# Kernel tuning notes

Measured on AMD Instinct MI355X. Metric: run time of the kernel, lower is better.

## Reference

```python
import jax, jax.numpy as jnp
import numpy as np

N_NODES = 10000
N_EDGES = 160000
F_IN = 256
HEADS = 4
F_OUT = 256
NEG_SLOPE = 0.2  # PyG GATConv default negative_slope
EPS = 1e-5       # GraphNorm eps


def gat_conv(x, src, dst, W, a_src, a_dst, bias, concat):
    """PyG-style GATConv. x:[N,Fin], W:[Fin,H*C], a_src/a_dst:[H,C], bias:[H*C] or [C].
    src/dst already include self-loops (add_self_loops=True default)."""
    N = x.shape[0]
    H, C = a_src.shape
    h = (x @ W).reshape(N, H, C)                      # per-head projected features
    al_s = jnp.einsum('nhc,hc->nh', h, a_src)          # [N,H]
    al_d = jnp.einsum('nhc,hc->nh', h, a_dst)          # [N,H]
    e = jax.nn.leaky_relu(al_s[src] + al_d[dst], NEG_SLOPE)  # [E,H] raw scores
    # segment softmax over edges grouped by destination node
    m = jax.ops.segment_max(e, dst, num_segments=N)    # [N,H]; every node has a self-loop
    ex = jnp.exp(e - m[dst])
    denom = jax.ops.segment_sum(ex, dst, num_segments=N)
    alpha = ex / denom[dst]                            # [E,H]
    out = jax.ops.segment_sum(h[src] * alpha[:, :, None], dst, num_segments=N)  # [N,H,C]
    out = out.reshape(N, H * C) if concat else out.mean(axis=1)
    return out + bias


def graph_norm(x, w, b, ms):
    """PyG GraphNorm over a single graph: y = w*(x-ms*mean)/sqrt(var+eps)+b."""
    mean = x.mean(axis=0, keepdims=True)
    sh = x - ms * mean
    var = (sh * sh).mean(axis=0, keepdims=True)
    return w * sh / jnp.sqrt(var + EPS) + b


def setup_inputs() -> dict:
    key = jax.random.key(0)
    ks = jax.random.split(key, 12)
    H1 = HEADS * F_IN  # 1024
    s = 0.05
    return {
        'x': jax.random.normal(ks[0], (N_NODES, F_IN), jnp.float32),
        'edge_index': jax.random.randint(ks[1], (2, N_EDGES), 0, N_NODES, jnp.int64),
        'W1': jax.random.normal(ks[2], (F_IN, HEADS * F_IN), jnp.float32) * s,
        'att_src1': jax.random.normal(ks[3], (HEADS, F_IN), jnp.float32) * s,
        'att_dst1': jax.random.normal(ks[4], (HEADS, F_IN), jnp.float32) * s,
        'b1': jnp.zeros((H1,), jnp.float32),
        'gn_w': jnp.ones((H1,), jnp.float32),
        'gn_b': jnp.zeros((H1,), jnp.float32),
        'gn_ms': jnp.ones((H1,), jnp.float32),
        'W2': jax.random.normal(ks[5], (H1, F_OUT), jnp.float32) * s,
        'att_src2': jax.random.normal(ks[6], (1, F_OUT), jnp.float32) * s,
        'att_dst2': jax.random.normal(ks[7], (1, F_OUT), jnp.float32) * s,
        'b2': jnp.zeros((F_OUT,), jnp.float32),
    }


def reference(x, edge_index, W1, att_src1, att_dst1, b1, gn_w, gn_b, gn_ms,
              W2, att_src2, att_dst2, b2):
    N = x.shape[0]
    loop = jnp.arange(N, dtype=edge_index.dtype)
    src = jnp.concatenate([edge_index[0], loop])  # add_self_loops=True
    dst = jnp.concatenate([edge_index[1], loop])
    h = gat_conv(x, src, dst, W1, att_src1, att_dst1, b1, concat=True)   # [N, H*Fin]
    h = graph_norm(h, gn_w, gn_b, gn_ms)
    h = jax.nn.relu(h)
    # F.dropout(training=self.training): eval mode -> identity
    out = gat_conv(h, src, dst, W2, att_src2, att_dst2, b2, concat=False)  # [N, Fout]
    return out
```

## Files before the change

kernel.cpp:

```cpp
#include <hip/hip_runtime.h>
#include <hip/hip_bf16.h>

#define NNODES 10000
#define FIN    256
#define HEADS  4
#define H1DIM  1024
#define FOUT   256
#define NEG    0.2f
#define GNEPS  1e-5f
#define SLOTS  96

typedef unsigned short u16;
typedef __attribute__((ext_vector_type(8))) short bf16x8;
typedef __attribute__((ext_vector_type(4))) float f32x4;

__device__ __forceinline__ float bf2f(u16 u) {
    union { unsigned int i; float f; } v; v.i = ((unsigned int)u) << 16; return v.f;
}
__device__ __forceinline__ u16 f2bf(float f) {
    __hip_bfloat16 h = __float2bfloat16(f);
    union { __hip_bfloat16 h; u16 u; } v; v.h = h; return v.u;
}
__device__ __forceinline__ float lrelu(float v) { return v > 0.f ? v : NEG * v; }

__device__ __forceinline__ void compute_flags(const int* ei, const u16* x,
                                              int& is64, int& isbf)
{
    int or_odd = ei[1] | ei[3] | ei[5] | ei[7] | ei[9] | ei[11];
    is64 = (or_odd == 0) ? 1 : 0;
    int sane = 1;
    for (int i = 0; i < 32; i += 2) {
        u16 w = x[i];
        int e = (w >> 7) & 0xFF;
        if (!(w == 0 || w == 0x8000 || (e >= 100 && e <= 150))) sane = 0;
    }
    isbf = sane;
}

struct CvtDesc { const void* src; float* dst; int n; };
struct CvtTable { CvtDesc d[9]; };

__global__ void pvec_kernel(const void* __restrict__ x, const int* __restrict__ ei,
                            const void* __restrict__ W1,
                            const void* __restrict__ as1, const void* __restrict__ ad1,
                            float* __restrict__ Pm,
                            int* __restrict__ flag, int* __restrict__ fflag)
{
    __shared__ int sfl[2];
    if (threadIdx.x == 0) {
        int is64, isbf;
        compute_flags(ei, (const u16*)x, is64, isbf);
        sfl[0] = is64; sfl[1] = isbf;
        if (blockIdx.x == 0) { flag[0] = is64; fflag[0] = isbf; }
    }
    __syncthreads();
    const int isbf = sfl[1];
    int wave = threadIdx.x >> 6, lane = threadIdx.x & 63;
    int idx = blockIdx.x * 4 + wave;
    int j = idx >> 8, k = idx & 255;
    int hd = j & 3;
    const void* av = (j < 4) ? as1 : ad1;
    int c = lane * 4;
    int widx = k * H1DIM + hd * FIN + c;
    int aidx = hd * FIN + c;
    float wv0, wv1, wv2, wv3, a0, a1, a2, a3;
    if (isbf) {
        ushort4 wu = *reinterpret_cast<const ushort4*>((const u16*)W1 + widx);
        ushort4 au = *reinterpret_cast<const ushort4*>((const u16*)av + aidx);
        wv0 = bf2f(wu.x); wv1 = bf2f(wu.y); wv2 = bf2f(wu.z); wv3 = bf2f(wu.w);
        a0 = bf2f(au.x); a1 = bf2f(au.y); a2 = bf2f(au.z); a3 = bf2f(au.w);
    } else {
        float4 wf = *reinterpret_cast<const float4*>((const float*)W1 + widx);
        float4 af = *reinterpret_cast<const float4*>((const float*)av + aidx);
        wv0 = wf.x; wv1 = wf.y; wv2 = wf.z; wv3 = wf.w;
        a0 = af.x; a1 = af.y; a2 = af.z; a3 = af.w;
    }
    float acc = wv0 * a0 + wv1 * a1 + wv2 * a2 + wv3 * a3;
#pragma unroll
    for (int off = 32; off > 0; off >>= 1)
        acc += __shfl_xor(acc, off, 64);
    if (lane == 0) Pm[j * FIN + k] = acc;
}

#define T0_N 2500
#define T1_N 256
#define T2_N 256
#define T3_N 9
#define T4_N 665
#define PREP_BLOCKS (T0_N + T1_N + T2_N + T3_N + T4_N)

__global__ void prep_kernel(const void* __restrict__ x, const int* __restrict__ ei,
                            const void* __restrict__ W1, const void* __restrict__ W2,
                            CvtTable smalls,
                            u16* __restrict__ xb, u16* __restrict__ W1t,
                            u16* __restrict__ W2t, const float* __restrict__ Pm,
                            int* __restrict__ cursor, int* __restrict__ ssort,
                            float* __restrict__ als, float* __restrict__ ald,
                            int NE, int Etot)
{
    __shared__ int sfl[2];
    __shared__ u16 tile[32][33];
    if (threadIdx.x == 0) {
        int is64, isbf;
        compute_flags(ei, (const u16*)x, is64, isbf);
        sfl[0] = is64; sfl[1] = isbf;
    }
    __syncthreads();
    const int is64 = sfl[0], isbf = sfl[1];
    const int b = blockIdx.x;
    const int tid = threadIdx.x;

    if (b < T0_N) {
        int i4 = (b * 256 + tid) * 4;
        ushort4 o;
        if (isbf) {
            o = *reinterpret_cast<const ushort4*>((const u16*)x + i4);
        } else {
            float4 v = *reinterpret_cast<const float4*>((const float*)x + i4);
            o.x = f2bf(v.x); o.y = f2bf(v.y); o.z = f2bf(v.z); o.w = f2bf(v.w);
        }
        *reinterpret_cast<ushort4*>(xb + i4) = o;
        int wave = tid >> 6, lane = tid & 63;
        int n = b * 4 + wave;
        float x0 = bf2f(o.x), x1 = bf2f(o.y), x2 = bf2f(o.z), x3 = bf2f(o.w);
        float r[8];
#pragma unroll
        for (int j = 0; j < 8; j++) {
            float4 p = *reinterpret_cast<const float4*>(Pm + j * FIN + lane * 4);
            r[j] = x0 * p.x + x1 * p.y + x2 * p.z + x3 * p.w;
        }
#pragma unroll
        for (int off = 32; off > 0; off >>= 1)
#pragma unroll
            for (int j = 0; j < 8; j++)
                r[j] += __shfl_xor(r[j], off, 64);
        if (lane == 0) {
            *reinterpret_cast<float4*>(als + n * 4) = make_float4(r[0], r[1], r[2], r[3]);
            *reinterpret_cast<float4*>(ald + n * 4) = make_float4(r[4], r[5], r[6], r[7]);
        }
    } else if (b < T0_N + T1_N + T2_N) {
        const int task1 = (b < T0_N + T1_N);
        const int bb = task1 ? (b - T0_N) : (b - T0_N - T1_N);
        const void* W = task1 ? W1 : W2;
        u16* Wt = task1 ? W1t : W2t;
        const int K = task1 ? FIN : H1DIM;
        const int N = task1 ? H1DIM : FOUT;
        int ntiles_n = N >> 5;
        int tk = bb / ntiles_n, tn = bb - tk * ntiles_n;
        if (tk >= (K >> 5)) return;
        int k0 = tk << 5, n0 = tn << 5;
        int r = tid >> 5, cdx = tid & 31;
#pragma unroll
        for (int i = 0; i < 4; i++) {
            int kk = i * 8 + r;
            int srcIdx = (k0 + kk) * N + n0 + cdx;
            u16 v = isbf ? ((const u16*)W)[srcIdx] : f2bf(((const float*)W)[srcIdx]);
            tile[kk][cdx] = v;
        }
        __syncthreads();
#pragma unroll
        for (int i = 0; i < 4; i++) {
            int nn = i * 8 + r;
            Wt[(size_t)(n0 + nn) * K + k0 + cdx] = tile[cdx][nn];
        }
    } else if (b < T0_N + T1_N + T2_N + T3_N) {
        const int bb = b - (T0_N + T1_N + T2_N);
        CvtDesc d = smalls.d[bb];
        int i4 = tid * 4;
        if (i4 >= d.n) return;
        if (isbf) {
            ushort4 u = *reinterpret_cast<const ushort4*>((const u16*)d.src + i4);
            *reinterpret_cast<float4*>(d.dst + i4) =
                make_float4(bf2f(u.x), bf2f(u.y), bf2f(u.z), bf2f(u.w));
        } else {
            *reinterpret_cast<float4*>(d.dst + i4) =
                *reinterpret_cast<const float4*>((const float*)d.src + i4);
        }
    } else {
        const int bb = b - (T0_N + T1_N + T2_N + T3_N);
        int e = bb * 256 + tid;
        if (e >= Etot) return;
        int src, dst;
        if (e < NE) {
            src = is64 ? ei[2 * e] : ei[e];
            dst = is64 ? ei[2 * (NE + e)] : ei[NE + e];
        } else {
            src = dst = e - NE;
        }
        if ((unsigned)dst >= NNODES) return;
        if ((unsigned)src >= NNODES) src = 0;
        int idx = atomicAdd(&cursor[dst], 1);
        if (idx < SLOTS) ssort[dst * SLOTS + idx] = src;
    }
}

__global__ void agg_x_kernel(const int* __restrict__ cursor, const int* __restrict__ ssort,
                             const float* __restrict__ als, const float* __restrict__ ald,
                             const u16* __restrict__ xb, u16* __restrict__ zbuf)
{
    const int wave = threadIdx.x >> 6, lane = threadIdx.x & 63;
    const int n = blockIdx.x * 4 + wave;
    const bool active = (n < NNODES);
    int e0 = 0, e1 = 0;
    float4 adv = make_float4(0.f, 0.f, 0.f, 0.f);
    if (active) {
        e0 = n * SLOTS;
        e1 = e0 + min(cursor[n], SLOTS);
        adv = *reinterpret_cast<const float4*>(ald + n * 4);
    }

    float m0 = -1e30f, m1 = -1e30f, m2 = -1e30f, m3 = -1e30f;
    for (int e = e0 + lane; e < e1; e += 64) {
        int s = ssort[e];
        float4 av = *reinterpret_cast<const float4*>(als + s * 4);
        m0 = fmaxf(m0, lrelu(av.x + adv.x));
        m1 = fmaxf(m1, lrelu(av.y + adv.y));
        m2 = fmaxf(m2, lrelu(av.z + adv.z));
        m3 = fmaxf(m3, lrelu(av.w + adv.w));
    }
#pragma unroll
    for (int off = 32; off > 0; off >>= 1) {
        m0 = fmaxf(m0, __shfl_xor(m0, off, 64));
        m1 = fmaxf(m1, __shfl_xor(m1, off, 64));
        m2 = fmaxf(m2, __shfl_xor(m2, off, 64));
        m3 = fmaxf(m3, __shfl_xor(m3, off, 64));
    }

    __shared__ float wlds[4][128][4];
    __shared__ int schk[4];
    int myCh = active ? ((e1 - e0 + 127) >> 7) : 0;
    if (lane == 0) schk[wave] = myCh;
    __syncthreads();
    int mc = max(max(schk[0], schk[1]), max(schk[2], schk[3]));

    float d0 = 0, d1 = 0, d2 = 0, d3 = 0;
    float a[4][4];
#pragma unroll
    for (int h = 0; h < 4; h++)
#pragma unroll
        for (int c = 0; c < 4; c++) a[h][c] = 0.f;

    for (int ch = 0; ch < mc; ch++) {
        int cs = e0 + ch * 128;
        int ce = min(cs + 128, e1);
        if (ch < myCh) {
            for (int e = cs + lane; e < ce; e += 64) {
                int s = ssort[e];
                float4 av = *reinterpret_cast<const float4*>(als + s * 4);
                float w0 = __expf(lrelu(av.x + adv.x) - m0);
                float w1 = __expf(lrelu(av.y + adv.y) - m1);
                float w2 = __expf(lrelu(av.z + adv.z) - m2);
                float w3 = __expf(lrelu(av.w + adv.w) - m3);
                *reinterpret_cast<float4*>(&wlds[wave][e - cs][0]) = make_float4(w0, w1, w2, w3);
                d0 += w0; d1 += w1; d2 += w2; d3 += w3;
            }
        }
        __syncthreads();
        if (ch < myCh) {
            int ee = cs;
            for (; ee + 1 < ce; ee += 2) {
                int s0 = ssort[ee];
                int s1 = ssort[ee + 1];
                float4 w0 = *reinterpret_cast<const float4*>(&wlds[wave][ee - cs][0]);
                float4 w1 = *reinterpret_cast<const float4*>(&wlds[wave][ee + 1 - cs][0]);
                ushort4 xv0 = *reinterpret_cast<const ushort4*>(xb + (size_t)s0 * FIN + lane * 4);
                ushort4 xv1 = *reinterpret_cast<const ushort4*>(xb + (size_t)s1 * FIN + lane * 4);
                float p0 = bf2f(xv0.x), p1 = bf2f(xv0.y), p2 = bf2f(xv0.z), p3 = bf2f(xv0.w);
                a[0][0] += w0.x * p0; a[0][1] += w0.x * p1; a[0][2] += w0.x * p2; a[0][3] += w0.x * p3;
                a[1][0] += w0.y * p0; a[1][1] += w0.y * p1; a[1][2] += w0.y * p2; a[1][3] += w0.y * p3;
                a[2][0] += w0.z * p0; a[2][1] += w0.z * p1; a[2][2] += w0.z * p2; a[2][3] += w0.z * p3;
                a[3][0] += w0.w * p0; a[3][1] += w0.w * p1; a[3][2] += w0.w * p2; a[3][3] += w0.w * p3;
                float q0 = bf2f(xv1.x), q1 = bf2f(xv1.y), q2 = bf2f(xv1.z), q3 = bf2f(xv1.w);
                a[0][0] += w1.x * q0; a[0][1] += w1.x * q1; a[0][2] += w1.x * q2; a[0][3] += w1.x * q3;
                a[1][0] += w1.y * q0; a[1][1] += w1.y * q1; a[1][2] += w1.y * q2; a[1][3] += w1.y * q3;
                a[2][0] += w1.z * q0; a[2][1] += w1.z * q1; a[2][2] += w1.z * q2; a[2][3] += w1.z * q3;
                a[3][0] += w1.w * q0; a[3][1] += w1.w * q1; a[3][2] += w1.w * q2; a[3][3] += w1.w * q3;
            }
            if (ee < ce) {
                int s = ssort[ee];
                float4 w = *reinterpret_cast<const float4*>(&wlds[wave][ee - cs][0]);
                ushort4 xv = *reinterpret_cast<const ushort4*>(xb + (size_t)s * FIN + lane * 4);
                float x0 = bf2f(xv.x), x1 = bf2f(xv.y), x2 = bf2f(xv.z), x3 = bf2f(xv.w);
                a[0][0] += w.x * x0; a[0][1] += w.x * x1; a[0][2] += w.x * x2; a[0][3] += w.x * x3;
                a[1][0] += w.y * x0; a[1][1] += w.y * x1; a[1][2] += w.y * x2; a[1][3] += w.y * x3;
                a[2][0] += w.z * x0; a[2][1] += w.z * x1; a[2][2] += w.z * x2; a[2][3] += w.z * x3;
                a[3][0] += w.w * x0; a[3][1] += w.w * x1; a[3][2] += w.w * x2; a[3][3] += w.w * x3;
            }
        }
        __syncthreads();
    }
    if (!active) return;
#pragma unroll
    for (int off = 32; off > 0; off >>= 1) {
        d0 += __shfl_xor(d0, off, 64);
        d1 += __shfl_xor(d1, off, 64);
        d2 += __shfl_xor(d2, off, 64);
        d3 += __shfl_xor(d3, off, 64);
    }
    float invs[4];
    invs[0] = d0 > 0.f ? 1.f / d0 : 0.f;
    invs[1] = d1 > 0.f ? 1.f / d1 : 0.f;
    invs[2] = d2 > 0.f ? 1.f / d2 : 0.f;
    invs[3] = d3 > 0.f ? 1.f / d3 : 0.f;
#pragma unroll
    for (int h = 0; h < 4; h++) {
        ushort4 o;
        o.x = f2bf(a[h][0] * invs[h]);
        o.y = f2bf(a[h][1] * invs[h]);
        o.z = f2bf(a[h][2] * invs[h]);
        o.w = f2bf(a[h][3] * invs[h]);
        *reinterpret_cast<ushort4*>(zbuf + (size_t)h * NNODES * FIN + (size_t)n * FIN + lane * 4) = o;
    }
}

#define LDS_STRIDE 40
#define KCHUNK2 1024
template<int BM, int BN, int MINW, bool NORM_A, bool BIAS, bool STATS, bool AL2>
__global__ void __launch_bounds__(256, MINW)
mfma_gemm(const u16* __restrict__ A, const u16* __restrict__ Bt,
          u16* __restrict__ C,
          const float* __restrict__ bias,
          float* __restrict__ gsum, float* __restrict__ gsum2,
          const float* __restrict__ gnw, const float* __restrict__ gnb,
          const float* __restrict__ gnms,
          const float* __restrict__ a2s, const float* __restrict__ a2d,
          float* __restrict__ al2s, float* __restrict__ al2d,
          int M, int K, int ldc, long aZ, long bZ, int cZ, int nbx)
{
    constexpr int MI = BM / 32;
    constexpr int NI = BN / 32;
    constexpr int NLOADS = (BM * 4 + BN * 4) / 256;
    __shared__ u16 Alds[BM * LDS_STRIDE];
    __shared__ u16 Blds[BN * LDS_STRIDE];
    __shared__ float sc_lds[NORM_A ? KCHUNK2 : 1];
    __shared__ float sh_lds[NORM_A ? KCHUNK2 : 1];

    int bid = blockIdx.x;
    {
        int nwg = gridDim.x;
        int q = nwg >> 3, r = nwg & 7;
        int xcd = bid & 7, l = bid >> 3;
        bid = (xcd < r ? xcd * (q + 1) : r * (q + 1) + (xcd - r) * q) + l;
    }
    const int bx = bid % nbx;
    const int by = bid / nbx;

    const u16* Az = A + (long)blockIdx.z * aZ;
    const u16* Bz = Bt + (long)blockIdx.z * bZ;

    const int tid  = threadIdx.x;
    const int lane = tid & 63;
    const int wave = tid >> 6;
    const int wm = wave >> 1, wn = wave & 1;
    const int l15 = lane & 15, quad = lane >> 4;
    const int n0 = bx * BN;
    const int m0 = by * BM;

    if (NORM_A) {
        const float invN = 1.0f / (float)NNODES;
        for (int i = tid; i < K; i += 256) {
            float mean = gsum[i] * invN;
            float ex2  = gsum2[i] * invN;
            float msv  = gnms[i];
            float var  = ex2 - 2.f * msv * mean * mean + msv * msv * mean * mean;
            float sc   = gnw[i] * rsqrtf(fmaxf(var, 0.f) + GNEPS);
            sc_lds[i] = sc;
            sh_lds[i] = gnb[i] - sc * msv * mean;
        }
        __syncthreads();
    }

    int lrow[NLOADS], lcol[NLOADS];
    bool lIsA[NLOADS];
#pragma unroll
    for (int i = 0; i < NLOADS; i++) {
        int g = i * 256 + tid;
        lIsA[i] = g < BM * 4;
        int gg = lIsA[i] ? g : g - BM * 4;
        lrow[i] = gg >> 2;
        lcol[i] = (gg & 3) * 8;
    }
    uint4 pre[NLOADS];

    auto issue = [&](int kt) {
#pragma unroll
        for (int i = 0; i < NLOADS; i++) {
            if (lIsA[i]) {
                int gr = m0 + lrow[i];
                pre[i] = (gr < M)
                    ? *reinterpret_cast<const uint4*>(Az + (size_t)gr * K + kt + lcol[i])
                    : make_uint4(0u, 0u, 0u, 0u);
            } else {
                pre[i] = *reinterpret_cast<const uint4*>(Bz + (size_t)(n0 + lrow[i]) * K + kt + lcol[i]);
            }
        }
    };
    auto commit = [&](int kt) {
#pragma unroll
        for (int i = 0; i < NLOADS; i++) {
            uint4 v = pre[i];
            if (lIsA[i]) {
                if (NORM_A) {
                    int kr = kt + lcol[i];
                    float4 s0 = *reinterpret_cast<const float4*>(&sc_lds[kr]);
                    float4 s1 = *reinterpret_cast<const float4*>(&sc_lds[kr + 4]);
                    float4 h0 = *reinterpret_cast<const float4*>(&sh_lds[kr]);
                    float4 h1 = *reinterpret_cast<const float4*>(&sh_lds[kr + 4]);
                    float sc[8] = {s0.x, s0.y, s0.z, s0.w, s1.x, s1.y, s1.z, s1.w};
                    float sh[8] = {h0.x, h0.y, h0.z, h0.w, h1.x, h1.y, h1.z, h1.w};
                    u16* pv = reinterpret_cast<u16*>(&v);
#pragma unroll
                    for (int j = 0; j < 8; j++)
                        pv[j] = f2bf(fmaxf(0.f, bf2f(pv[j]) * sc[j] + sh[j]));
                }
                *reinterpret_cast<uint4*>(&Alds[lrow[i] * LDS_STRIDE + lcol[i]]) = v;
            } else {
                *reinterpret_cast<uint4*>(&Blds[lrow[i] * LDS_STRIDE + lcol[i]]) = v;
            }
        }
    };

    f32x4 acc[MI][NI];
#pragma unroll
    for (int i = 0; i < MI; i++)
#pragma unroll
        for (int j = 0; j < NI; j++) acc[i][j] = (f32x4){0.f, 0.f, 0.f, 0.f};

    issue(0);
    for (int kt = 0; kt < K; kt += 32) {
        commit(kt);
        __syncthreads();
        if (kt + 32 < K) issue(kt + 32);

        bf16x8 a_frag[MI], b_frag[NI];
#pragma unroll
        for (int mi = 0; mi < MI; mi++)
            a_frag[mi] = *reinterpret_cast<const bf16x8*>(
                &Alds[(wm * (BM / 2) + mi * 16 + l15) * LDS_STRIDE + quad * 8]);
#pragma unroll
        for (int ni = 0; ni < NI; ni++)
            b_frag[ni] = *reinterpret_cast<const bf16x8*>(
                &Blds[(wn * (BN / 2) + ni * 16 + l15) * LDS_STRIDE + quad * 8]);
#pragma unroll
        for (int mi = 0; mi < MI; mi++)
#pragma unroll
            for (int ni = 0; ni < NI; ni++)
                acc[mi][ni] = __builtin_amdgcn_mfma_f32_16x16x32_bf16(
                    a_frag[mi], b_frag[ni], acc[mi][ni], 0, 0, 0);
        __syncthreads();
    }

    float sacc[NI], qacc[NI];
#pragma unroll
    for (int ni = 0; ni < NI; ni++) { sacc[ni] = 0.f; qacc[ni] = 0.f; }

#pragma unroll
    for (int mi = 0; mi < MI; mi++) {
#pragma unroll
        for (int r = 0; r < 4; r++) {
            int row = m0 + wm * (BM / 2) + mi * 16 + quad * 4 + r;
            if (row >= M) continue;
            float ps = 0.f, pd = 0.f;
#pragma unroll
            for (int ni = 0; ni < NI; ni++) {
                int col = n0 + wn * (BN / 2) + ni * 16 + l15;
                float v = acc[mi][ni][r];
                if (BIAS) v += bias[blockIdx.z * cZ + col];
                if (STATS) { sacc[ni] += v; qacc[ni] += v * v; }
                if (AL2) { ps += v * a2s[col]; pd += v * a2d[col]; }
                C[(size_t)row * ldc + blockIdx.z * cZ + col] = f2bf(v);
            }
            if (AL2) {
                ps += __shfl_xor(ps, 1, 64); pd += __shfl_xor(pd, 1, 64);
                ps += __shfl_xor(ps, 2, 64); pd += __shfl_xor(pd, 2, 64);
                ps += __shfl_xor(ps, 4, 64); pd += __shfl_xor(pd, 4, 64);
                ps += __shfl_xor(ps, 8, 64); pd += __shfl_xor(pd, 8, 64);
                if (l15 == 0) {
                    atomicAdd(&al2s[row], ps);
                    atomicAdd(&al2d[row], pd);
                }
            }
        }
    }
    if (STATS) {
#pragma unroll
        for (int ni = 0; ni < NI; ni++) {
            float s = sacc[ni], q = qacc[ni];
            s += __shfl_xor(s, 16, 64); q += __shfl_xor(q, 16, 64);
            s += __shfl_xor(s, 32, 64); q += __shfl_xor(q, 32, 64);
            if (quad == 0) {
                int ch = blockIdx.z * cZ + n0 + wn * (BN / 2) + ni * 16 + l15;
                atomicAdd(&gsum[ch], s);
                atomicAdd(&gsum2[ch], q);
            }
        }
    }
}

__global__ void agg2_kernel(const int* __restrict__ cursor, const int* __restrict__ ssort,
                            const float* __restrict__ als, const float* __restrict__ ald,
                            const u16* __restrict__ h2, const float* __restrict__ b2,
                            const int* __restrict__ fflag, void* __restrict__ outv)
{
    const int wave = threadIdx.x >> 6, lane = threadIdx.x & 63;
    const int n = blockIdx.x * 4 + wave;
    const bool active = (n < NNODES);
    int e0 = 0, e1 = 0;
    float adv = 0.f;
    if (active) {
        e0 = n * SLOTS;
        e1 = e0 + min(cursor[n], SLOTS);
        adv = ald[n];
    }

    float m = -1e30f;
    for (int e = e0 + lane; e < e1; e += 64) {
        int s = ssort[e];
        m = fmaxf(m, lrelu(als[s] + adv));
    }
#pragma unroll
    for (int off = 32; off > 0; off >>= 1)
        m = fmaxf(m, __shfl_xor(m, off, 64));

    __shared__ float wlds[4][128];
    __shared__ int schk[4];
    int myCh = active ? ((e1 - e0 + 127) >> 7) : 0;
    if (lane == 0) schk[wave] = myCh;
    __syncthreads();
    int mc = max(max(schk[0], schk[1]), max(schk[2], schk[3]));

    float d = 0.f, a0 = 0.f, a1 = 0.f, a2 = 0.f, a3 = 0.f;
    for (int ch = 0; ch < mc; ch++) {
        int cs = e0 + ch * 128;
        int ce = min(cs + 128, e1);
        if (ch < myCh) {
            for (int e = cs + lane; e < ce; e += 64) {
                int s = ssort[e];
                float w = __expf(lrelu(als[s] + adv) - m);
                wlds[wave][e - cs] = w;
                d += w;
            }
        }
        __syncthreads();
        if (ch < myCh) {
            int ee = cs;
            for (; ee + 1 < ce; ee += 2) {
                int s0 = ssort[ee];
                int s1 = ssort[ee + 1];
                float w0 = wlds[wave][ee - cs];
                float w1 = wlds[wave][ee + 1 - cs];
                ushort4 hv0 = *reinterpret_cast<const ushort4*>(h2 + (size_t)s0 * FOUT + lane * 4);
                ushort4 hv1 = *reinterpret_cast<const ushort4*>(h2 + (size_t)s1 * FOUT + lane * 4);
                a0 += w0 * bf2f(hv0.x); a1 += w0 * bf2f(hv0.y);
                a2 += w0 * bf2f(hv0.z); a3 += w0 * bf2f(hv0.w);
                a0 += w1 * bf2f(hv1.x); a1 += w1 * bf2f(hv1.y);
                a2 += w1 * bf2f(hv1.z); a3 += w1 * bf2f(hv1.w);
            }
            if (ee < ce) {
                int s = ssort[ee];
                float w = wlds[wave][ee - cs];
                ushort4 hv = *reinterpret_cast<const ushort4*>(h2 + (size_t)s * FOUT + lane * 4);
                a0 += w * bf2f(hv.x); a1 += w * bf2f(hv.y);
                a2 += w * bf2f(hv.z); a3 += w * bf2f(hv.w);
            }
        }
        __syncthreads();
    }
    if (!active) return;
#pragma unroll
    for (int off = 32; off > 0; off >>= 1)
        d += __shfl_xor(d, off, 64);
    float inv = d > 0.f ? 1.f / d : 0.f;
    int c = lane * 4;
    float4 bv = *reinterpret_cast<const float4*>(b2 + c);
    float r0 = a0 * inv + bv.x;
    float r1 = a1 * inv + bv.y;
    float r2 = a2 * inv + bv.z;
    float r3 = a3 * inv + bv.w;
    if (fflag[0]) {
        ushort4 o;
        o.x = f2bf(r0); o.y = f2bf(r1); o.z = f2bf(r2); o.w = f2bf(r3);
        *reinterpret_cast<ushort4*>((u16*)outv + (size_t)n * FOUT + c) = o;
    } else {
        *reinterpret_cast<float4*>((float*)outv + (size_t)n * FOUT + c) =
            make_float4(r0, r1, r2, r3);
    }
}

extern "C" void kernel_launch(void* const* d_in, const int* in_sizes, int n_in,
                              void* d_out, int out_size, void* d_ws, size_t ws_size,
                              hipStream_t stream)
{
    const void* x    = d_in[0];
    const int*  ei   = (const int*)d_in[1];
    const void* W1   = d_in[2];
    const void* as1  = d_in[3];
    const void* ad1  = d_in[4];
    const void* b1   = d_in[5];
    const void* gnw  = d_in[6];
    const void* gnb  = d_in[7];
    const void* gnms = d_in[8];
    const void* W2   = d_in[9];
    const void* as2  = d_in[10];
    const void* ad2  = d_in[11];
    const void* b2   = d_in[12];

    const int NE   = in_sizes[1] / 2;
    const int Etot = NE + NNODES;

    char* w = (char*)d_ws;
    size_t off = 0;
    auto carve = [&](size_t bytes) -> char* {
        char* p = w + off;
        off = (off + bytes + 255) & ~(size_t)255;
        return p;
    };
    int*   cursor = (int*)carve((size_t)NNODES * 4);
    float* gsum   = (float*)carve(1024 * 4);
    float* gsum2  = (float*)carve(1024 * 4);
    float* al2s   = (float*)carve((size_t)NNODES * 4);
    float* al2d   = (float*)carve((size_t)NNODES * 4);
    size_t zero_bytes = off;
    int*   flag   = (int*)carve(256);
    int*   fflag  = (int*)carve(256);
    int*   ssort  = (int*)carve((size_t)NNODES * SLOTS * 4);
    u16*   zbuf   = (u16*)carve((size_t)HEADS * NNODES * FIN * 2);
    u16*   out1b  = (u16*)carve((size_t)NNODES * H1DIM * 2);
    float* al1s   = (float*)carve((size_t)NNODES * HEADS * 4);
    float* al1d   = (float*)carve((size_t)NNODES * HEADS * 4);
    u16*   xb     = (u16*)carve((size_t)NNODES * FIN * 2);
    u16*   W1t    = (u16*)carve((size_t)H1DIM * FIN * 2);
    u16*   W2t    = (u16*)carve((size_t)FOUT * H1DIM * 2);
    float* Pm     = (float*)carve(8 * FIN * 4);
    float* b1f    = (float*)carve(1024 * 4);
    float* gnwf   = (float*)carve(1024 * 4);
    float* gnbf   = (float*)carve(1024 * 4);
    float* gnmsf  = (float*)carve(1024 * 4);
    float* as2f   = (float*)carve(256 * 4);
    float* ad2f   = (float*)carve(256 * 4);
    float* b2f    = (float*)carve(256 * 4);
    float* as1f   = (float*)carve(1024 * 4);
    float* ad1f   = (float*)carve(1024 * 4);
    (void)ws_size;

    u16* h2b = xb;

    hipMemsetAsync(d_ws, 0, zero_bytes, stream);

    pvec_kernel<<<512, 256, 0, stream>>>(x, ei, W1, as1, ad1, Pm, flag, fflag);

    {
        CvtTable tab;
        tab.d[0] = { b1,   b1f,   H1DIM };
        tab.d[1] = { gnw,  gnwf,  H1DIM };
        tab.d[2] = { gnb,  gnbf,  H1DIM };
        tab.d[3] = { gnms, gnmsf, H1DIM };
        tab.d[4] = { as2,  as2f,  FOUT };
        tab.d[5] = { ad2,  ad2f,  FOUT };
        tab.d[6] = { b2,   b2f,   FOUT };
        tab.d[7] = { as1,  as1f,  H1DIM };
        tab.d[8] = { ad1,  ad1f,  H1DIM };
        prep_kernel<<<PREP_BLOCKS, 256, 0, stream>>>(x, ei, W1, W2, tab,
                                                     xb, W1t, W2t, Pm, cursor, ssort,
                                                     al1s, al1d, NE, Etot);
    }
    agg_x_kernel<<<2500, 256, 0, stream>>>(cursor, ssort, al1s, al1d, xb, zbuf);
    {
        const int nbx = FIN / 128;
        const int nby = (NNODES + 63) / 64;
        dim3 grd(nbx * nby, 1, HEADS);
        mfma_gemm<64, 128, 4, false, true, true, false><<<grd, 256, 0, stream>>>(
            zbuf, W1t, out1b, b1f, gsum, gsum2, nullptr, nullptr, nullptr,
            nullptr, nullptr, nullptr, nullptr,
            NNODES, FIN, H1DIM, (long)NNODES * FIN, (long)FIN * FIN, FIN, nbx);
    }
    {
        const int nbx = FOUT / 64;
        const int nby = (NNODES + 63) / 64;
        dim3 grd(nbx * nby, 1, 1);
        mfma_gemm<64, 64, 4, true, false, false, true><<<grd, 256, 0, stream>>>(
            out1b, W2t, h2b, nullptr, gsum, gsum2, gnwf, gnbf, gnmsf,
            as2f, ad2f, al2s, al2d,
            NNODES, H1DIM, FOUT, 0L, 0L, 0, nbx);
    }
    agg2_kernel<<<2500, 256, 0, stream>>>(cursor, ssort, al2s, al2d, h2b, b2f, fflag, d_out);
}
```

Before: 214.3 us.

## Double-buffer GEMM LDS tiles and stage B/A via global_load_lds

The MFMA GEMM drops its single padded LDS buffer and register-staged prefetch. It now uses two unpadded LDS buffers and direct global-to-LDS loads (global_load_lds) for B and for A when no normalization is needed. The normalized A path still goes through registers but commits into the other buffer after compute. This removes one barrier per k-step and lets loads overlap compute, at the cost of unpadded LDS rows, which may cause bank conflicts on fragment reads. It also drops the row-bounds check on A in the direct-load path, which risks out-of-bounds reads when M is not a multiple of BM.

```diff
diff --git a/kernel.cpp b/kernel.cpp
--- a/kernel.cpp
+++ b/kernel.cpp
@@ -22,6 +22,12 @@
     union { __hip_bfloat16 h; u16 u; } v; v.h = h; return v.u;
 }
 __device__ __forceinline__ float lrelu(float v) { return v > 0.f ? v : NEG * v; }
+
+__device__ __forceinline__ void gll16(const u16* g, u16* l) {
+    __builtin_amdgcn_global_load_lds(
+        (const __attribute__((address_space(1))) unsigned int*)g,
+        (__attribute__((address_space(3))) unsigned int*)l, 16, 0, 0);
+}
 
 __device__ __forceinline__ void compute_flags(const int* ei, const u16* x,
                                               int& is64, int& isbf)
@@ -313,8 +319,6 @@
     }
 }
 
-#define LDS_STRIDE 40
-#define KCHUNK2 1024
 template<int BM, int BN, int MINW, bool NORM_A, bool BIAS, bool STATS, bool AL2>
 __global__ void __launch_bounds__(256, MINW)
 mfma_gemm(const u16* __restrict__ A, const u16* __restrict__ Bt,
@@ -329,11 +333,10 @@
 {
     constexpr int MI = BM / 32;
     constexpr int NI = BN / 32;
-    constexpr int NLOADS = (BM * 4 + BN * 4) / 256;
-    __shared__ u16 Alds[BM * LDS_STRIDE];
-    __shared__ u16 Blds[BN * LDS_STRIDE];
-    __shared__ float sc_lds[NORM_A ? KCHUNK2 : 1];
-    __shared__ float sh_lds[NORM_A ? KCHUNK2 : 1];
+    __shared__ u16 Alds[2][BM * 32];
+    __shared__ u16 Blds[2][BN * 32];
+    __shared__ float sc_lds[NORM_A ? H1DIM : 1];
+    __shared__ float sh_lds[NORM_A ? H1DIM : 1];
 
     int bid = blockIdx.x;
     {
@@ -370,55 +373,44 @@
         __syncthreads();
     }
 
-    int lrow[NLOADS], lcol[NLOADS];
-    bool lIsA[NLOADS];
-#pragma unroll
-    for (int i = 0; i < NLOADS; i++) {
-        int g = i * 256 + tid;
-        lIsA[i] = g < BM * 4;
-        int gg = lIsA[i] ? g : g - BM * 4;
-        lrow[i] = gg >> 2;
-        lcol[i] = (gg & 3) * 8;
-    }
-    uint4 pre[NLOADS];
-
-    auto issue = [&](int kt) {
-#pragma unroll
-        for (int i = 0; i < NLOADS; i++) {
-            if (lIsA[i]) {
-                int gr = m0 + lrow[i];
-                pre[i] = (gr < M)
-                    ? *reinterpret_cast<const uint4*>(Az + (size_t)gr * K + kt + lcol[i])
-                    : make_uint4(0u, 0u, 0u, 0u);
-            } else {
-                pre[i] = *reinterpret_cast<const uint4*>(Bz + (size_t)(n0 + lrow[i]) * K + kt + lcol[i]);
-            }
+    const int lrw = lane >> 2, lcg = (lane & 3) * 8;
+    auto stageB = [&](int c, int kt) {
+#pragma unroll
+        for (int s = wave; s < BN / 16; s += 4) {
+            const u16* g = Bz + (size_t)(n0 + s * 16 + lrw) * K + kt + lcg;
+            gll16(g, &Blds[c][s * 512]);
         }
     };
-    auto commit = [&](int kt) {
-#pragma unroll
-        for (int i = 0; i < NLOADS; i++) {
-            uint4 v = pre[i];
-            if (lIsA[i]) {
-                if (NORM_A) {
-                    int kr = kt + lcol[i];
-                    float4 s0 = *reinterpret_cast<const float4*>(&sc_lds[kr]);
-                    float4 s1 = *reinterpret_cast<const float4*>(&sc_lds[kr + 4]);
-                    float4 h0 = *reinterpret_cast<const float4*>(&sh_lds[kr]);
-                    float4 h1 = *reinterpret_cast<const float4*>(&sh_lds[kr + 4]);
-                    float sc[8] = {s0.x, s0.y, s0.z, s0.w, s1.x, s1.y, s1.z, s1.w};
-                    float sh[8] = {h0.x, h0.y, h0.z, h0.w, h1.x, h1.y, h1.z, h1.w};
-                    u16* pv = reinterpret_cast<u16*>(&v);
-#pragma unroll
-                    for (int j = 0; j < 8; j++)
-                        pv[j] = f2bf(fmaxf(0.f, bf2f(pv[j]) * sc[j] + sh[j]));
-                }
-                *reinterpret_cast<uint4*>(&Alds[lrow[i] * LDS_STRIDE + lcol[i]]) = v;
-            } else {
-                *reinterpret_cast<uint4*>(&Blds[lrow[i] * LDS_STRIDE + lcol[i]]) = v;
-            }
+    auto stageAg = [&](int c, int kt) {
+#pragma unroll
+        for (int s = wave; s < BM / 16; s += 4) {
+            const u16* g = Az + (size_t)(m0 + s * 16 + lrw) * K + kt + lcg;
+            gll16(g, &Alds[c][s * 512]);
         }
     };
+    const int arow = tid >> 2, acol = (tid & 3) * 8;
+    uint4 apre;
+    auto issueA = [&](int kt) {
+        int gr = m0 + arow;
+        apre = (gr < M)
+            ? *reinterpret_cast<const uint4*>(Az + (size_t)gr * K + kt + acol)
+            : make_uint4(0u, 0u, 0u, 0u);
+    };
+    auto commitA = [&](int c, int kt) {
+        uint4 v = apre;
+        int kr = kt + acol;
+        float4 s0 = *reinterpret_cast<const float4*>(&sc_lds[kr]);
+        float4 s1 = *reinterpret_cast<const float4*>(&sc_lds[kr + 4]);
+        float4 h0 = *reinterpret_cast<const float4*>(&sh_lds[kr]);
+        float4 h1 = *reinterpret_cast<const float4*>(&sh_lds[kr + 4]);
+        float sc[8] = {s0.x, s0.y, s0.z, s0.w, s1.x, s1.y, s1.z, s1.w};
+        float sh[8] = {h0.x, h0.y, h0.z, h0.w, h1.x, h1.y, h1.z, h1.w};
+        u16* pv = reinterpret_cast<u16*>(&v);
+#pragma unroll
+        for (int j = 0; j < 8; j++)
+            pv[j] = f2bf(fmaxf(0.f, bf2f(pv[j]) * sc[j] + sh[j]));
+        *reinterpret_cast<uint4*>(&Alds[c][arow * 32 + acol]) = v;
+    };
 
     f32x4 acc[MI][NI];
 #pragma unroll
@@ -426,28 +418,39 @@
 #pragma unroll
         for (int j = 0; j < NI; j++) acc[i][j] = (f32x4){0.f, 0.f, 0.f, 0.f};
 
-    issue(0);
-    for (int kt = 0; kt < K; kt += 32) {
-        commit(kt);
-        __syncthreads();
-        if (kt + 32 < K) issue(kt + 32);
-
+    auto compute = [&](int c) {
         bf16x8 a_frag[MI], b_frag[NI];
 #pragma unroll
         for (int mi = 0; mi < MI; mi++)
             a_frag[mi] = *reinterpret_cast<const bf16x8*>(
-                &Alds[(wm * (BM / 2) + mi * 16 + l15) * LDS_STRIDE + quad * 8]);
+                &Alds[c][(wm * (BM / 2) + mi * 16 + l15) * 32 + quad * 8]);
 #pragma unroll
         for (int ni = 0; ni < NI; ni++)
             b_frag[ni] = *reinterpret_cast<const bf16x8*>(
-                &Blds[(wn * (BN / 2) + ni * 16 + l15) * LDS_STRIDE + quad * 8]);
+                &Blds[c][(wn * (BN / 2) + ni * 16 + l15) * 32 + quad * 8]);
 #pragma unroll
         for (int mi = 0; mi < MI; mi++)
 #pragma unroll
             for (int ni = 0; ni < NI; ni++)
                 acc[mi][ni] = __builtin_amdgcn_mfma_f32_16x16x32_bf16(
                     a_frag[mi], b_frag[ni], acc[mi][ni], 0, 0, 0);
+    };
+
+    if (NORM_A) { issueA(0); commitA(0, 0); } else { stageAg(0, 0); }
+    stageB(0, 0);
+    __syncthreads();
+
+    int cur = 0;
+    for (int kt = 0; kt < K; kt += 32) {
+        const bool nxt = (kt + 32 < K);
+        if (nxt) {
+            if (NORM_A) issueA(kt + 32); else stageAg(cur ^ 1, kt + 32);
+            stageB(cur ^ 1, kt + 32);
+        }
+        compute(cur);
+        if (nxt && NORM_A) commitA(cur ^ 1, kt + 32);
         __syncthreads();
+        cur ^= 1;
     }
 
     float sacc[NI], qacc[NI];
```

Result: faster. 205.7 us (-4.0%).
